# Kernel optimization log

Hardware: AMD Instinct MI355X
Metric: run time of the kernel (lower is better)

The kernel has to match this reference:

```python
import jax, jax.numpy as jnp
import numpy as np
import math

D_MODEL = 512
N_HEADS = 8
MAX_SEQ_LEN = 4096
DENSITY = 0.3


def _make_random_mask(key, seq_len, density=DENSITY):
    # rand < density, symmetrized via (m + m.T)/2, clamped to [0,1], diag = 1
    u = jax.random.uniform(key, (seq_len, seq_len), dtype=jnp.float32)
    m = (u < density).astype(jnp.float32)
    m = jnp.clip((m + m.T) * 0.5, 0.0, 1.0)
    return m.at[jnp.diag_indices(seq_len)].set(1.0)


def setup_inputs() -> dict:
    key = jax.random.key(0)
    ks = jax.random.split(key, 10)
    B, T, C = 2, 4096, D_MODEL
    scale = 1.0 / math.sqrt(C)
    x = jax.random.normal(ks[0], (B, T, C), dtype=jnp.float32)
    mask = _make_random_mask(ks[1], MAX_SEQ_LEN)[:T, :T]
    # Linear weights stored as (in, out): y = x @ W + b
    Wq = jax.random.normal(ks[2], (C, C), dtype=jnp.float32) * scale
    Wk = jax.random.normal(ks[3], (C, C), dtype=jnp.float32) * scale
    Wv = jax.random.normal(ks[4], (C, C), dtype=jnp.float32) * scale
    Wo = jax.random.normal(ks[5], (C, C), dtype=jnp.float32) * scale
    bq = jax.random.normal(ks[6], (C,), dtype=jnp.float32) * scale
    bk = jax.random.normal(ks[7], (C,), dtype=jnp.float32) * scale
    bv = jax.random.normal(ks[8], (C,), dtype=jnp.float32) * scale
    bo = jax.random.normal(ks[9], (C,), dtype=jnp.float32) * scale
    return {"x": x, "mask": mask, "Wq": Wq, "bq": bq, "Wk": Wk, "bk": bk,
            "Wv": Wv, "bv": bv, "Wo": Wo, "bo": bo}


def reference(x, mask, Wq, bq, Wk, bk, Wv, bv, Wo, bo):
    B, T, C = x.shape
    H = N_HEADS
    dk = C // H
    q = (x @ Wq + bq).reshape(B, T, H, dk)
    k = (x @ Wk + bk).reshape(B, T, H, dk)
    v = (x @ Wv + bv).reshape(B, T, H, dk)
    # scores: [B, H, T, T]
    attn = jnp.einsum('bthd,bshd->bhts', q, k) / math.sqrt(dk)
    attn = attn * mask[None, None, :, :]  # multiplicative mask PRE-softmax
    p = jax.nn.softmax(attn, axis=-1)
    out = jnp.einsum('bhts,bshd->bthd', p, v).reshape(B, T, C)
    return out @ Wo + bo
```

## Files before the change

kernel.cpp:

```cpp
#include <hip/hip_runtime.h>
#include <math.h>

#define D_MODEL 512
#define N_HEADS 8
#define DK 64

typedef __attribute__((ext_vector_type(8))) short short8;
typedef __attribute__((ext_vector_type(4))) float f32x4;

typedef __attribute__((address_space(1))) const unsigned as1_uint;
typedef __attribute__((address_space(3))) unsigned as3_uint;

__device__ __forceinline__ unsigned short f2bf(float f) {
    unsigned u = __builtin_bit_cast(unsigned, f);
    u = (u + 0x7fff + ((u >> 16) & 1)) >> 16;
    return (unsigned short)u;
}

__global__ __launch_bounds__(256) void cvt_x_kernel(const float* __restrict__ x,
                                                    unsigned short* __restrict__ xb, int n8)
{
    int i = blockIdx.x * 256 + threadIdx.x;
    if (i >= n8) return;
    float4 a = ((const float4*)x)[i * 2];
    float4 b = ((const float4*)x)[i * 2 + 1];
    short8 o;
    o[0] = f2bf(a.x); o[1] = f2bf(a.y); o[2] = f2bf(a.z); o[3] = f2bf(a.w);
    o[4] = f2bf(b.x); o[5] = f2bf(b.y); o[6] = f2bf(b.z); o[7] = f2bf(b.w);
    ((short8*)xb)[i] = o;
}

__global__ __launch_bounds__(256) void cvt_mask_kernel(const float* __restrict__ m,
                                                       unsigned char* __restrict__ mu, int n4)
{
    int i = blockIdx.x * 256 + threadIdx.x;
    if (i >= n4) return;
    float4 v = ((const float4*)m)[i];
    uchar4 o = { (unsigned char)(v.x * 2.0f + 0.5f),
                 (unsigned char)(v.y * 2.0f + 0.5f),
                 (unsigned char)(v.z * 2.0f + 0.5f),
                 (unsigned char)(v.w * 2.0f + 0.5f) };
    ((uchar4*)mu)[i] = o;
}

__global__ __launch_bounds__(256) void cvt_wt_kernel(const float* __restrict__ W,
                                                     unsigned short* __restrict__ Wt)
{
    __shared__ float tile[64][65];
    int t = threadIdx.x;
    int c0 = blockIdx.x * 64;
    int r0 = blockIdx.y * 64;
    #pragma unroll
    for (int i = 0; i < 16; i++) {
        int e = i * 256 + t, r = e >> 6, c = e & 63;
        tile[c][r] = W[(size_t)(r0 + r) * D_MODEL + c0 + c];
    }
    __syncthreads();
    #pragma unroll
    for (int i = 0; i < 16; i++) {
        int e = i * 256 + t, n = e >> 6, kk = e & 63;
        Wt[(size_t)(c0 + n) * D_MODEL + r0 + kk] = f2bf(tile[n][kk]);
    }
}

template<int MODE>
__global__ __launch_bounds__(512) void gemm_mfma_kernel(
    const unsigned short* __restrict__ A, const unsigned short* __restrict__ Bt,
    const float* __restrict__ bias, void* __restrict__ outp, int M, int T)
{
    constexpr int K = D_MODEL;
    __shared__ unsigned short As[2][128 * 32];
    __shared__ unsigned short Bs[2][128 * 32];
    int t = threadIdx.x;
    int lane = t & 63, w = t >> 6;
    int ql = lane & 15, kg = lane >> 4;
    int m0 = blockIdx.y * 128, n0 = blockIdx.x * 128;
    int wm = w >> 2, wn = w & 3;

    const unsigned short* srcA = A + (size_t)(m0 + (t >> 2)) * K + (t & 3) * 8;
    const unsigned short* srcB = Bt + (size_t)(n0 + (t >> 2)) * K + (t & 3) * 8;

    f32x4 acc[4][2];
    #pragma unroll
    for (int i = 0; i < 4; i++)
        #pragma unroll
        for (int j = 0; j < 2; j++) { f32x4 z = {0.f, 0.f, 0.f, 0.f}; acc[i][j] = z; }

    constexpr int NIT = K / 32;
    int cur = 0;
    __builtin_amdgcn_global_load_lds((as1_uint*)(srcA),
        (as3_uint*)((char*)&As[0][0] + w * 1024), 16, 0, 0);
    __builtin_amdgcn_global_load_lds((as1_uint*)(srcB),
        (as3_uint*)((char*)&Bs[0][0] + w * 1024), 16, 0, 0);
    __syncthreads();

    for (int it = 0; it < NIT; ++it) {
        if (it + 1 < NIT) {
            int k0 = (it + 1) * 32;
            __builtin_amdgcn_global_load_lds((as1_uint*)(srcA + k0),
                (as3_uint*)((char*)&As[cur ^ 1][0] + w * 1024), 16, 0, 0);
            __builtin_amdgcn_global_load_lds((as1_uint*)(srcB + k0),
                (as3_uint*)((char*)&Bs[cur ^ 1][0] + w * 1024), 16, 0, 0);
        }
        short8 af[4], bfr[2];
        #pragma unroll
        for (int fm = 0; fm < 4; fm++)
            af[fm] = *(const short8*)((const char*)&As[cur][0] + (wm * 64 + fm * 16 + ql) * 64 + kg * 16);
        #pragma unroll
        for (int fn = 0; fn < 2; fn++)
            bfr[fn] = *(const short8*)((const char*)&Bs[cur][0] + (wn * 32 + fn * 16 + ql) * 64 + kg * 16);
        #pragma unroll
        for (int fm = 0; fm < 4; fm++)
            #pragma unroll
            for (int fn = 0; fn < 2; fn++) {
                if (MODE == 3)
                    acc[fm][fn] = __builtin_amdgcn_mfma_f32_16x16x32_bf16(bfr[fn], af[fm], acc[fm][fn], 0, 0, 0);
                else
                    acc[fm][fn] = __builtin_amdgcn_mfma_f32_16x16x32_bf16(af[fm], bfr[fn], acc[fm][fn], 0, 0, 0);
            }
        __syncthreads();
        cur ^= 1;
    }

    #pragma unroll
    for (int fm = 0; fm < 4; fm++) {
        #pragma unroll
        for (int fn = 0; fn < 2; fn++) {
            if (MODE == 3) {
                int m = m0 + wm * 64 + fm * 16 + ql;
                int b = m / T, tt = m % T;
                #pragma unroll
                for (int r = 0; r < 4; r++) {
                    int n = n0 + wn * 32 + fn * 16 + kg * 4 + r;
                    float val = acc[fm][fn][r] + bias[n];
                    int h = n >> 6, d = n & 63;
                    ((unsigned short*)outp)[((size_t)(b * N_HEADS + h) * DK + d) * T + tt] = f2bf(val);
                }
            } else {
                int n = n0 + wn * 32 + fn * 16 + ql;
                float bn = bias[n];
                #pragma unroll
                for (int r = 0; r < 4; r++) {
                    int m = m0 + wm * 64 + fm * 16 + kg * 4 + r;
                    float val = acc[fm][fn][r] + bn;
                    if (MODE == 0) {
                        ((float*)outp)[(size_t)m * D_MODEL + n] = val;
                    } else {
                        if (MODE == 1) val *= 0.0625f * 1.44269504089f;
                        int b = m / T, tt = m % T;
                        int h = n >> 6, d = n & 63;
                        ((unsigned short*)outp)[((size_t)(b * N_HEADS + h) * T + tt) * DK + d] = f2bf(val);
                    }
                }
            }
        }
    }
}

__global__ __launch_bounds__(256) void attn_mfma_kernel(
    const unsigned short* __restrict__ q, const unsigned short* __restrict__ k,
    const unsigned short* __restrict__ v, const unsigned char* __restrict__ mu,
    unsigned short* __restrict__ out, int B, int T)
{
    __shared__ unsigned short Ks[2][64 * 64];
    __shared__ unsigned short Vt[2][64 * 64];
    __shared__ unsigned short Ps[4][32 * 64];

    int t = threadIdx.x;
    int lane = t & 63, w = t >> 6;
    int ql = lane & 15, kg = lane >> 4;
    int bh = blockIdx.x;
    int qt = blockIdx.y;
    int h = bh & (N_HEADS - 1), b = bh >> 3;
    int qr0 = qt * 128;

    const char* kbase = (const char*)(k + (size_t)bh * T * DK);
    const char* vbase = (const char*)(v + (size_t)bh * DK * T);

    int lin0 = w * 1024 + lane * 16;
    int lin1 = 4096 + lin0;
    int row0 = lin0 >> 7, row1 = lin1 >> 7;
    int sw0 = (row0 & 7) << 4, sw1 = (row1 & 7) << 4;
    const char* gK0 = kbase + (lin0 ^ sw0);
    const char* gK1 = kbase + (lin1 ^ sw1);
    const char* gV0 = vbase + (size_t)row0 * (2 * T) + ((lin0 & 127) ^ sw0);
    const char* gV1 = vbase + (size_t)row1 * (2 * T) + ((lin1 & 127) ^ sw1);

    short8 qfr[2][2];
    #pragma unroll
    for (int qf = 0; qf < 2; qf++) {
        const unsigned short* qrow = q + ((size_t)bh * T + qr0 + w * 32 + qf * 16 + ql) * DK + kg * 8;
        qfr[qf][0] = *(const short8*)(qrow);
        qfr[qf][1] = *(const short8*)(qrow + 32);
    }

    const unsigned char* mrow0 = mu + (size_t)(qr0 + w * 32 + ql) * T + kg * 4;
    const unsigned char* mrow1 = mrow0 + (size_t)16 * T;

    f32x4 oacc[2][4];
    #pragma unroll
    for (int qf = 0; qf < 2; qf++)
        #pragma unroll
        for (int c = 0; c < 4; c++) { f32x4 z = {0.f, 0.f, 0.f, 0.f}; oacc[qf][c] = z; }
    float lacc0 = 0.f, lacc1 = 0.f;

    unsigned mcur0[4], mcur1[4];
    #pragma unroll
    for (int c = 0; c < 4; c++) {
        mcur0[c] = *(const unsigned*)(mrow0 + c * 16);
        mcur1[c] = *(const unsigned*)(mrow1 + c * 16);
    }
    __builtin_amdgcn_global_load_lds((as1_uint*)gK0, (as3_uint*)((char*)&Ks[0][0] + w * 1024), 16, 0, 0);
    __builtin_amdgcn_global_load_lds((as1_uint*)gK1, (as3_uint*)((char*)&Ks[0][0] + 4096 + w * 1024), 16, 0, 0);
    __builtin_amdgcn_global_load_lds((as1_uint*)gV0, (as3_uint*)((char*)&Vt[0][0] + w * 1024), 16, 0, 0);
    __builtin_amdgcn_global_load_lds((as1_uint*)gV1, (as3_uint*)((char*)&Vt[0][0] + 4096 + w * 1024), 16, 0, 0);

    int ntiles = T / 64;
    for (int kt = 0; kt < ntiles; kt++) {
        __syncthreads();
        int cur = kt & 1;
        bool havenext = (kt + 1) < ntiles;

        unsigned mnxt0[4], mnxt1[4];
        if (havenext) {
            const unsigned char* mp0 = mrow0 + (size_t)(kt + 1) * 64;
            const unsigned char* mp1 = mrow1 + (size_t)(kt + 1) * 64;
            #pragma unroll
            for (int c = 0; c < 4; c++) {
                mnxt0[c] = *(const unsigned*)(mp0 + c * 16);
                mnxt1[c] = *(const unsigned*)(mp1 + c * 16);
            }
            size_t ko = (size_t)(kt + 1) * 8192;
            size_t vo = (size_t)(kt + 1) * 128;
            __builtin_amdgcn_global_load_lds((as1_uint*)(gK0 + ko),
                (as3_uint*)((char*)&Ks[cur ^ 1][0] + w * 1024), 16, 0, 0);
            __builtin_amdgcn_global_load_lds((as1_uint*)(gK1 + ko),
                (as3_uint*)((char*)&Ks[cur ^ 1][0] + 4096 + w * 1024), 16, 0, 0);
            __builtin_amdgcn_global_load_lds((as1_uint*)(gV0 + vo),
                (as3_uint*)((char*)&Vt[cur ^ 1][0] + w * 1024), 16, 0, 0);
            __builtin_amdgcn_global_load_lds((as1_uint*)(gV1 + vo),
                (as3_uint*)((char*)&Vt[cur ^ 1][0] + 4096 + w * 1024), 16, 0, 0);
        }

        f32x4 sacc[2][4];
        #pragma unroll
        for (int qf = 0; qf < 2; qf++)
            #pragma unroll
            for (int c = 0; c < 4; c++) { f32x4 z = {0.f, 0.f, 0.f, 0.f}; sacc[qf][c] = z; }
        __builtin_amdgcn_s_setprio(1);
        #pragma unroll
        for (int ks = 0; ks < 2; ks++) {
            #pragma unroll
            for (int c = 0; c < 4; c++) {
                int row = c * 16 + ql;
                short8 kf = *(const short8*)((const char*)&Ks[cur][0] +
                            ((row * 128 + ks * 64 + kg * 16) ^ ((row & 7) << 4)));
                sacc[0][c] = __builtin_amdgcn_mfma_f32_16x16x32_bf16(kf, qfr[0][ks], sacc[0][c], 0, 0, 0);
                sacc[1][c] = __builtin_amdgcn_mfma_f32_16x16x32_bf16(kf, qfr[1][ks], sacc[1][c], 0, 0, 0);
            }
        }
        __builtin_amdgcn_s_setprio(0);

        #pragma unroll
        for (int c = 0; c < 4; c++) {
            unsigned mw = mcur0[c];
            float p0 = __builtin_amdgcn_exp2f(sacc[0][c][0] * (float)(mw & 0xffu));
            float p1 = __builtin_amdgcn_exp2f(sacc[0][c][1] * (float)((mw >> 8) & 0xffu));
            float p2 = __builtin_amdgcn_exp2f(sacc[0][c][2] * (float)((mw >> 16) & 0xffu));
            float p3 = __builtin_amdgcn_exp2f(sacc[0][c][3] * (float)(mw >> 24));
            lacc0 += (p0 + p1) + (p2 + p3);
            unsigned lo, hi;
            asm("v_cvt_pk_bf16_f32 %0, %1, %2" : "=v"(lo) : "v"(p0), "v"(p1));
            asm("v_cvt_pk_bf16_f32 %0, %1, %2" : "=v"(hi) : "v"(p2), "v"(p3));
            int byteoff = (ql * 128 + (c * 16 + kg * 4) * 2) ^ ((ql & 7) << 4);
            uint2 pr = { lo, hi };
            *(uint2*)((char*)&Ps[w][0] + byteoff) = pr;

            unsigned nw = mcur1[c];
            float q0 = __builtin_amdgcn_exp2f(sacc[1][c][0] * (float)(nw & 0xffu));
            float q1 = __builtin_amdgcn_exp2f(sacc[1][c][1] * (float)((nw >> 8) & 0xffu));
            float q2 = __builtin_amdgcn_exp2f(sacc[1][c][2] * (float)((nw >> 16) & 0xffu));
            float q3 = __builtin_amdgcn_exp2f(sacc[1][c][3] * (float)(nw >> 24));
            lacc1 += (q0 + q1) + (q2 + q3);
            unsigned lo1, hi1;
            asm("v_cvt_pk_bf16_f32 %0, %1, %2" : "=v"(lo1) : "v"(q0), "v"(q1));
            asm("v_cvt_pk_bf16_f32 %0, %1, %2" : "=v"(hi1) : "v"(q2), "v"(q3));
            uint2 pr1 = { lo1, hi1 };
            *(uint2*)((char*)&Ps[w][0] + 2048 + byteoff) = pr1;
        }

        __builtin_amdgcn_s_setprio(1);
        #pragma unroll
        for (int ks = 0; ks < 2; ks++) {
            int pboff = (ql * 128 + ks * 64 + kg * 16) ^ ((ql & 7) << 4);
            short8 pa0 = *(const short8*)((const char*)&Ps[w][0] + pboff);
            short8 pa1 = *(const short8*)((const char*)&Ps[w][0] + 2048 + pboff);
            #pragma unroll
            for (int c2 = 0; c2 < 4; c2++) {
                int rowd = c2 * 16 + ql;
                short8 vb = *(const short8*)((const char*)&Vt[cur][0] +
                            ((rowd * 128 + ks * 64 + kg * 16) ^ ((rowd & 7) << 4)));
                oacc[0][c2] = __builtin_amdgcn_mfma_f32_16x16x32_bf16(pa0, vb, oacc[0][c2], 0, 0, 0);
                oacc[1][c2] = __builtin_amdgcn_mfma_f32_16x16x32_bf16(pa1, vb, oacc[1][c2], 0, 0, 0);
            }
        }
        __builtin_amdgcn_s_setprio(0);

        if (havenext) {
            #pragma unroll
            for (int c = 0; c < 4; c++) { mcur0[c] = mnxt0[c]; mcur1[c] = mnxt1[c]; }
        }
    }

    lacc0 += __shfl_xor(lacc0, 16, 64);
    lacc0 += __shfl_xor(lacc0, 32, 64);
    lacc1 += __shfl_xor(lacc1, 16, 64);
    lacc1 += __shfl_xor(lacc1, 32, 64);
    #pragma unroll
    for (int qf = 0; qf < 2; qf++) {
        float la = qf ? lacc1 : lacc0;
        #pragma unroll
        for (int r = 0; r < 4; r++) {
            float linv = 1.0f / __shfl(la, kg * 4 + r, 64);
            size_t rowo = ((size_t)b * T + qr0 + w * 32 + qf * 16 + kg * 4 + r) * D_MODEL + h * DK;
            #pragma unroll
            for (int c2 = 0; c2 < 4; c2++)
                out[rowo + c2 * 16 + ql] = f2bf(oacc[qf][c2][r] * linv);
        }
    }
}

extern "C" void kernel_launch(void* const* d_in, const int* in_sizes, int n_in,
                              void* d_out, int out_size, void* d_ws, size_t ws_size,
                              hipStream_t stream) {
    const float* x    = (const float*)d_in[0];
    const float* mask = (const float*)d_in[1];
    const float* Wq   = (const float*)d_in[2];
    const float* bq   = (const float*)d_in[3];
    const float* Wk   = (const float*)d_in[4];
    const float* bk   = (const float*)d_in[5];
    const float* Wv   = (const float*)d_in[6];
    const float* bv   = (const float*)d_in[7];
    const float* Wo   = (const float*)d_in[8];
    const float* bo   = (const float*)d_in[9];

    int T = (int)(sqrt((double)in_sizes[1]) + 0.5);
    int C = D_MODEL;
    int B = in_sizes[0] / (T * C);
    int M = B * T;

    size_t MK = (size_t)M * C;
    unsigned short* xb  = (unsigned short*)d_ws;
    unsigned short* Wtq = xb + MK;
    unsigned short* Wtk = Wtq + (size_t)C * C;
    unsigned short* Wtv = Wtk + (size_t)C * C;
    unsigned short* Wto = Wtv + (size_t)C * C;
    unsigned short* qb  = Wto + (size_t)C * C;
    unsigned short* kb  = qb + MK;
    unsigned short* vb  = kb + MK;
    unsigned short* attb = vb + MK;
    unsigned char*  mu  = (unsigned char*)(attb + MK);

    int n8 = (int)(MK / 8);
    cvt_x_kernel<<<(n8 + 255) / 256, 256, 0, stream>>>(x, xb, n8);
    int n4 = T * T / 4;
    cvt_mask_kernel<<<(n4 + 255) / 256, 256, 0, stream>>>(mask, mu, n4);
    dim3 wtg(C / 64, C / 64, 1);
    cvt_wt_kernel<<<wtg, 256, 0, stream>>>(Wq, Wtq);
    cvt_wt_kernel<<<wtg, 256, 0, stream>>>(Wk, Wtk);
    cvt_wt_kernel<<<wtg, 256, 0, stream>>>(Wv, Wtv);
    cvt_wt_kernel<<<wtg, 256, 0, stream>>>(Wo, Wto);

    dim3 gg(C / 128, M / 128, 1);
    gemm_mfma_kernel<1><<<gg, 512, 0, stream>>>(xb, Wtq, bq, qb, M, T);
    gemm_mfma_kernel<2><<<gg, 512, 0, stream>>>(xb, Wtk, bk, kb, M, T);
    gemm_mfma_kernel<3><<<gg, 512, 0, stream>>>(xb, Wtv, bv, vb, M, T);

    dim3 ga(B * N_HEADS, T / 128, 1);
    attn_mfma_kernel<<<ga, 256, 0, stream>>>(qb, kb, vb, mu, attb, B, T);

    gemm_mfma_kernel<0><<<gg, 512, 0, stream>>>(attb, Wto, bo, d_out, M, T);
}
```

Baseline: 225.1 us.

## Split attention KV range across two blocks, fuse QKV GEMMs, defer PV

Fuses the three Q/K/V projection GEMMs into one launch. This relies on the Wtq/Wtk/Wtv buffers sitting next to each other in the workspace, so they act as one 1536-wide weight. Splits the attention key range into two halves along a new grid dimension, which doubles the block count from 512 to 1024 for better CU occupancy. Each half writes unnormalized fp32 partial outputs and row sums, and a new merge kernel combines and normalizes them. The V tile is now single-buffered and the PV product is software-pipelined one tile behind QK. The cost is extra fp32 partial traffic (about 16MB written and read back) and one additional launch.

After: 258.0 us. +14.6%, slower.

```diff
diff --git a/kernel.cpp b/kernel.cpp
--- a/kernel.cpp
+++ b/kernel.cpp
@@ -4,6 +4,7 @@
 #define D_MODEL 512
 #define N_HEADS 8
 #define DK 64
+#define QSCALE (0.0625f * 1.44269504089f)
 
 typedef __attribute__((ext_vector_type(8))) short short8;
 typedef __attribute__((ext_vector_type(4))) float f32x4;
@@ -63,10 +64,11 @@
     }
 }
 
-template<int MODE>
-__global__ __launch_bounds__(512) void gemm_mfma_kernel(
-    const unsigned short* __restrict__ A, const unsigned short* __restrict__ Bt,
-    const float* __restrict__ bias, void* __restrict__ outp, int M, int T)
+__global__ __launch_bounds__(512) void gemm_qkv_kernel(
+    const unsigned short* __restrict__ A, const unsigned short* __restrict__ Wt,
+    const float* __restrict__ bq, const float* __restrict__ bk, const float* __restrict__ bv,
+    unsigned short* __restrict__ qb, unsigned short* __restrict__ kb,
+    unsigned short* __restrict__ vb, int M, int T)
 {
     constexpr int K = D_MODEL;
     __shared__ unsigned short As[2][128 * 32];
@@ -76,9 +78,10 @@
     int ql = lane & 15, kg = lane >> 4;
     int m0 = blockIdx.y * 128, n0 = blockIdx.x * 128;
     int wm = w >> 2, wn = w & 3;
+    bool vmode = (n0 >= 1024);
 
     const unsigned short* srcA = A + (size_t)(m0 + (t >> 2)) * K + (t & 3) * 8;
-    const unsigned short* srcB = Bt + (size_t)(n0 + (t >> 2)) * K + (t & 3) * 8;
+    const unsigned short* srcB = Wt + (size_t)(n0 + (t >> 2)) * K + (t & 3) * 8;
 
     f32x4 acc[4][2];
     #pragma unroll
@@ -109,15 +112,19 @@
         #pragma unroll
         for (int fn = 0; fn < 2; fn++)
             bfr[fn] = *(const short8*)((const char*)&Bs[cur][0] + (wn * 32 + fn * 16 + ql) * 64 + kg * 16);
-        #pragma unroll
-        for (int fm = 0; fm < 4; fm++)
-            #pragma unroll
-            for (int fn = 0; fn < 2; fn++) {
-                if (MODE == 3)
+        if (vmode) {
+            #pragma unroll
+            for (int fm = 0; fm < 4; fm++)
+                #pragma unroll
+                for (int fn = 0; fn < 2; fn++)
                     acc[fm][fn] = __builtin_amdgcn_mfma_f32_16x16x32_bf16(bfr[fn], af[fm], acc[fm][fn], 0, 0, 0);
-                else
+        } else {
+            #pragma unroll
+            for (int fm = 0; fm < 4; fm++)
+                #pragma unroll
+                for (int fn = 0; fn < 2; fn++)
                     acc[fm][fn] = __builtin_amdgcn_mfma_f32_16x16x32_bf16(af[fm], bfr[fn], acc[fm][fn], 0, 0, 0);
-            }
+        }
         __syncthreads();
         cur ^= 1;
     }
@@ -126,32 +133,100 @@
     for (int fm = 0; fm < 4; fm++) {
         #pragma unroll
         for (int fn = 0; fn < 2; fn++) {
-            if (MODE == 3) {
+            if (vmode) {
                 int m = m0 + wm * 64 + fm * 16 + ql;
                 int b = m / T, tt = m % T;
                 #pragma unroll
                 for (int r = 0; r < 4; r++) {
-                    int n = n0 + wn * 32 + fn * 16 + kg * 4 + r;
-                    float val = acc[fm][fn][r] + bias[n];
+                    int n = (n0 - 1024) + wn * 32 + fn * 16 + kg * 4 + r;
+                    float val = acc[fm][fn][r] + bv[n];
                     int h = n >> 6, d = n & 63;
-                    ((unsigned short*)outp)[((size_t)(b * N_HEADS + h) * DK + d) * T + tt] = f2bf(val);
+                    vb[((size_t)(b * N_HEADS + h) * DK + d) * T + tt] = f2bf(val);
                 }
             } else {
                 int n = n0 + wn * 32 + fn * 16 + ql;
-                float bn = bias[n];
+                int nn = n & 511;
+                bool isq = (n0 < 512);
+                float bn = isq ? bq[nn] : bk[nn];
+                unsigned short* dst = isq ? qb : kb;
+                int h = nn >> 6, d = nn & 63;
                 #pragma unroll
                 for (int r = 0; r < 4; r++) {
                     int m = m0 + wm * 64 + fm * 16 + kg * 4 + r;
+                    int b = m / T, tt = m % T;
                     float val = acc[fm][fn][r] + bn;
-                    if (MODE == 0) {
-                        ((float*)outp)[(size_t)m * D_MODEL + n] = val;
-                    } else {
-                        if (MODE == 1) val *= 0.0625f * 1.44269504089f;
-                        int b = m / T, tt = m % T;
-                        int h = n >> 6, d = n & 63;
-                        ((unsigned short*)outp)[((size_t)(b * N_HEADS + h) * T + tt) * DK + d] = f2bf(val);
-                    }
+                    if (isq) val *= QSCALE;
+                    dst[((size_t)(b * N_HEADS + h) * T + tt) * DK + d] = f2bf(val);
                 }
+            }
+        }
+    }
+}
+
+__global__ __launch_bounds__(512) void gemm_out_kernel(
+    const unsigned short* __restrict__ A, const unsigned short* __restrict__ Bt,
+    const float* __restrict__ bias, float* __restrict__ outp, int M)
+{
+    constexpr int K = D_MODEL;
+    __shared__ unsigned short As[2][128 * 32];
+    __shared__ unsigned short Bs[2][128 * 32];
+    int t = threadIdx.x;
+    int lane = t & 63, w = t >> 6;
+    int ql = lane & 15, kg = lane >> 4;
+    int m0 = blockIdx.y * 128, n0 = blockIdx.x * 128;
+    int wm = w >> 2, wn = w & 3;
+
+    const unsigned short* srcA = A + (size_t)(m0 + (t >> 2)) * K + (t & 3) * 8;
+    const unsigned short* srcB = Bt + (size_t)(n0 + (t >> 2)) * K + (t & 3) * 8;
+
+    f32x4 acc[4][2];
+    #pragma unroll
+    for (int i = 0; i < 4; i++)
+        #pragma unroll
+        for (int j = 0; j < 2; j++) { f32x4 z = {0.f, 0.f, 0.f, 0.f}; acc[i][j] = z; }
+
+    constexpr int NIT = K / 32;
+    int cur = 0;
+    __builtin_amdgcn_global_load_lds((as1_uint*)(srcA),
+        (as3_uint*)((char*)&As[0][0] + w * 1024), 16, 0, 0);
+    __builtin_amdgcn_global_load_lds((as1_uint*)(srcB),
+        (as3_uint*)((char*)&Bs[0][0] + w * 1024), 16, 0, 0);
+    __syncthreads();
+
+    for (int it = 0; it < NIT; ++it) {
+        if (it + 1 < NIT) {
+            int k0 = (it + 1) * 32;
+            __builtin_amdgcn_global_load_lds((as1_uint*)(srcA + k0),
+                (as3_uint*)((char*)&As[cur ^ 1][0] + w * 1024), 16, 0, 0);
+            __builtin_amdgcn_global_load_lds((as1_uint*)(srcB + k0),
+                (as3_uint*)((char*)&Bs[cur ^ 1][0] + w * 1024), 16, 0, 0);
+        }
+        short8 af[4], bfr[2];
+        #pragma unroll
+        for (int fm = 0; fm < 4; fm++)
+            af[fm] = *(const short8*)((const char*)&As[cur][0] + (wm * 64 + fm * 16 + ql) * 64 + kg * 16);
+        #pragma unroll
+        for (int fn = 0; fn < 2; fn++)
+            bfr[fn] = *(const short8*)((const char*)&Bs[cur][0] + (wn * 32 + fn * 16 + ql) * 64 + kg * 16);
+        #pragma unroll
+        for (int fm = 0; fm < 4; fm++)
+            #pragma unroll
+            for (int fn = 0; fn < 2; fn++)
+                acc[fm][fn] = __builtin_amdgcn_mfma_f32_16x16x32_bf16(af[fm], bfr[fn], acc[fm][fn], 0, 0, 0);
+        __syncthreads();
+        cur ^= 1;
+    }
+
+    #pragma unroll
+    for (int fm = 0; fm < 4; fm++) {
+        #pragma unroll
+        for (int fn = 0; fn < 2; fn++) {
+            int n = n0 + wn * 32 + fn * 16 + ql;
+            float bn = bias[n];
+            #pragma unroll
+            for (int r = 0; r < 4; r++) {
+                int m = m0 + wm * 64 + fm * 16 + kg * 4 + r;
+                outp[(size_t)m * D_MODEL + n] = acc[fm][fn][r] + bn;
             }
         }
     }
@@ -160,22 +235,25 @@
 __global__ __launch_bounds__(256) void attn_mfma_kernel(
     const unsigned short* __restrict__ q, const unsigned short* __restrict__ k,
     const unsigned short* __restrict__ v, const unsigned char* __restrict__ mu,
-    unsigned short* __restrict__ out, int B, int T)
+    float* __restrict__ opart, float* __restrict__ lpart, int B, int T)
 {
     __shared__ unsigned short Ks[2][64 * 64];
-    __shared__ unsigned short Vt[2][64 * 64];
+    __shared__ unsigned short Vt[64 * 64];
     __shared__ unsigned short Ps[4][32 * 64];
 
     int t = threadIdx.x;
     int lane = t & 63, w = t >> 6;
     int ql = lane & 15, kg = lane >> 4;
-    int bh = blockIdx.x;
-    int qt = blockIdx.y;
+    int bh = blockIdx.x, qt = blockIdx.y, z = blockIdx.z;
     int h = bh & (N_HEADS - 1), b = bh >> 3;
     int qr0 = qt * 128;
-
-    const char* kbase = (const char*)(k + (size_t)bh * T * DK);
-    const char* vbase = (const char*)(v + (size_t)bh * DK * T);
+    int Th = T >> 1;
+    int kv0 = z * Th;
+    int nt = Th / 64;
+    int M = B * T;
+
+    const char* kbase = (const char*)(k + ((size_t)bh * T + kv0) * DK);
+    const char* vbase = (const char*)(v + (size_t)bh * DK * T + kv0);
 
     int lin0 = w * 1024 + lane * 16;
     int lin1 = 4096 + lin0;
@@ -194,14 +272,14 @@
         qfr[qf][1] = *(const short8*)(qrow + 32);
     }
 
-    const unsigned char* mrow0 = mu + (size_t)(qr0 + w * 32 + ql) * T + kg * 4;
+    const unsigned char* mrow0 = mu + (size_t)(qr0 + w * 32 + ql) * T + kv0 + kg * 4;
     const unsigned char* mrow1 = mrow0 + (size_t)16 * T;
 
     f32x4 oacc[2][4];
     #pragma unroll
     for (int qf = 0; qf < 2; qf++)
         #pragma unroll
-        for (int c = 0; c < 4; c++) { f32x4 z = {0.f, 0.f, 0.f, 0.f}; oacc[qf][c] = z; }
+        for (int c = 0; c < 4; c++) { f32x4 zz = {0.f, 0.f, 0.f, 0.f}; oacc[qf][c] = zz; }
     float lacc0 = 0.f, lacc1 = 0.f;
 
     unsigned mcur0[4], mcur1[4];
@@ -212,14 +290,11 @@
     }
     __builtin_amdgcn_global_load_lds((as1_uint*)gK0, (as3_uint*)((char*)&Ks[0][0] + w * 1024), 16, 0, 0);
     __builtin_amdgcn_global_load_lds((as1_uint*)gK1, (as3_uint*)((char*)&Ks[0][0] + 4096 + w * 1024), 16, 0, 0);
-    __builtin_amdgcn_global_load_lds((as1_uint*)gV0, (as3_uint*)((char*)&Vt[0][0] + w * 1024), 16, 0, 0);
-    __builtin_amdgcn_global_load_lds((as1_uint*)gV1, (as3_uint*)((char*)&Vt[0][0] + 4096 + w * 1024), 16, 0, 0);
-
-    int ntiles = T / 64;
-    for (int kt = 0; kt < ntiles; kt++) {
+
+    for (int kt = 0; kt < nt; kt++) {
         __syncthreads();
         int cur = kt & 1;
-        bool havenext = (kt + 1) < ntiles;
+        bool havenext = (kt + 1) < nt;
 
         unsigned mnxt0[4], mnxt1[4];
         if (havenext) {
@@ -231,22 +306,48 @@
                 mnxt1[c] = *(const unsigned*)(mp1 + c * 16);
             }
             size_t ko = (size_t)(kt + 1) * 8192;
-            size_t vo = (size_t)(kt + 1) * 128;
             __builtin_amdgcn_global_load_lds((as1_uint*)(gK0 + ko),
                 (as3_uint*)((char*)&Ks[cur ^ 1][0] + w * 1024), 16, 0, 0);
             __builtin_amdgcn_global_load_lds((as1_uint*)(gK1 + ko),
                 (as3_uint*)((char*)&Ks[cur ^ 1][0] + 4096 + w * 1024), 16, 0, 0);
+        }
+
+        if (kt > 0) {
+            __builtin_amdgcn_s_setprio(1);
+            #pragma unroll
+            for (int ks = 0; ks < 2; ks++) {
+                int pboff = (ql * 128 + ks * 64 + kg * 16) ^ ((ql & 7) << 4);
+                short8 pa0 = *(const short8*)((const char*)&Ps[w][0] + pboff);
+                short8 pa1 = *(const short8*)((const char*)&Ps[w][0] + 2048 + pboff);
+                #pragma unroll
+                for (int c2 = 0; c2 < 4; c2++) {
+                    int rowd = c2 * 16 + ql;
+                    short8 vb = *(const short8*)((const char*)Vt +
+                                ((rowd * 128 + ks * 64 + kg * 16) ^ ((rowd & 7) << 4)));
+                    oacc[0][c2] = __builtin_amdgcn_mfma_f32_16x16x32_bf16(pa0, vb, oacc[0][c2], 0, 0, 0);
+                    oacc[1][c2] = __builtin_amdgcn_mfma_f32_16x16x32_bf16(pa1, vb, oacc[1][c2], 0, 0, 0);
+                }
+            }
+            __builtin_amdgcn_s_setprio(0);
+        }
+
+        __builtin_amdgcn_sched_barrier(0);
+        __builtin_amdgcn_s_barrier();
+        __builtin_amdgcn_sched_barrier(0);
+
+        {
+            size_t vo = (size_t)kt * 128;
             __builtin_amdgcn_global_load_lds((as1_uint*)(gV0 + vo),
-                (as3_uint*)((char*)&Vt[cur ^ 1][0] + w * 1024), 16, 0, 0);
+                (as3_uint*)((char*)Vt + w * 1024), 16, 0, 0);
             __builtin_amdgcn_global_load_lds((as1_uint*)(gV1 + vo),
-                (as3_uint*)((char*)&Vt[cur ^ 1][0] + 4096 + w * 1024), 16, 0, 0);
+                (as3_uint*)((char*)Vt + 4096 + w * 1024), 16, 0, 0);
         }
 
         f32x4 sacc[2][4];
         #pragma unroll
         for (int qf = 0; qf < 2; qf++)
             #pragma unroll
-            for (int c = 0; c < 4; c++) { f32x4 z = {0.f, 0.f, 0.f, 0.f}; sacc[qf][c] = z; }
+            for (int c = 0; c < 4; c++) { f32x4 zz = {0.f, 0.f, 0.f, 0.f}; sacc[qf][c] = zz; }
         __builtin_amdgcn_s_setprio(1);
         #pragma unroll
         for (int ks = 0; ks < 2; ks++) {
@@ -289,45 +390,74 @@
             *(uint2*)((char*)&Ps[w][0] + 2048 + byteoff) = pr1;
         }
 
-        __builtin_amdgcn_s_setprio(1);
-        #pragma unroll
-        for (int ks = 0; ks < 2; ks++) {
-            int pboff = (ql * 128 + ks * 64 + kg * 16) ^ ((ql & 7) << 4);
-            short8 pa0 = *(const short8*)((const char*)&Ps[w][0] + pboff);
-            short8 pa1 = *(const short8*)((const char*)&Ps[w][0] + 2048 + pboff);
-            #pragma unroll
-            for (int c2 = 0; c2 < 4; c2++) {
-                int rowd = c2 * 16 + ql;
-                short8 vb = *(const short8*)((const char*)&Vt[cur][0] +
-                            ((rowd * 128 + ks * 64 + kg * 16) ^ ((rowd & 7) << 4)));
-                oacc[0][c2] = __builtin_amdgcn_mfma_f32_16x16x32_bf16(pa0, vb, oacc[0][c2], 0, 0, 0);
-                oacc[1][c2] = __builtin_amdgcn_mfma_f32_16x16x32_bf16(pa1, vb, oacc[1][c2], 0, 0, 0);
-            }
-        }
-        __builtin_amdgcn_s_setprio(0);
-
         if (havenext) {
             #pragma unroll
             for (int c = 0; c < 4; c++) { mcur0[c] = mnxt0[c]; mcur1[c] = mnxt1[c]; }
         }
     }
+
+    __syncthreads();
+    __builtin_amdgcn_s_setprio(1);
+    #pragma unroll
+    for (int ks = 0; ks < 2; ks++) {
+        int pboff = (ql * 128 + ks * 64 + kg * 16) ^ ((ql & 7) << 4);
+        short8 pa0 = *(const short8*)((const char*)&Ps[w][0] + pboff);
+        short8 pa1 = *(const short8*)((const char*)&Ps[w][0] + 2048 + pboff);
+        #pragma unroll
+        for (int c2 = 0; c2 < 4; c2++) {
+            int rowd = c2 * 16 + ql;
+            short8 vb = *(const short8*)((const char*)Vt +
+                        ((rowd * 128 + ks * 64 + kg * 16) ^ ((rowd & 7) << 4)));
+            oacc[0][c2] = __builtin_amdgcn_mfma_f32_16x16x32_bf16(pa0, vb, oacc[0][c2], 0, 0, 0);
+            oacc[1][c2] = __builtin_amdgcn_mfma_f32_16x16x32_bf16(pa1, vb, oacc[1][c2], 0, 0, 0);
+        }
+    }
+    __builtin_amdgcn_s_setprio(0);
 
     lacc0 += __shfl_xor(lacc0, 16, 64);
     lacc0 += __shfl_xor(lacc0, 32, 64);
     lacc1 += __shfl_xor(lacc1, 16, 64);
     lacc1 += __shfl_xor(lacc1, 32, 64);
+    if (kg == 0) {
+        lpart[((size_t)z * 16 + bh) * T + qr0 + w * 32 + ql] = lacc0;
+        lpart[((size_t)z * 16 + bh) * T + qr0 + w * 32 + 16 + ql] = lacc1;
+    }
     #pragma unroll
     for (int qf = 0; qf < 2; qf++) {
-        float la = qf ? lacc1 : lacc0;
         #pragma unroll
         for (int r = 0; r < 4; r++) {
-            float linv = 1.0f / __shfl(la, kg * 4 + r, 64);
-            size_t rowo = ((size_t)b * T + qr0 + w * 32 + qf * 16 + kg * 4 + r) * D_MODEL + h * DK;
+            size_t rowo = ((size_t)z * M + (size_t)b * T + qr0 + w * 32 + qf * 16 + kg * 4 + r) * D_MODEL + h * DK;
+            f32x4* oa = &oacc[qf][0];
             #pragma unroll
             for (int c2 = 0; c2 < 4; c2++)
-                out[rowo + c2 * 16 + ql] = f2bf(oacc[qf][c2][r] * linv);
-        }
-    }
+                opart[rowo + c2 * 16 + ql] = oa[c2][r];
+        }
+    }
+}
+
+__global__ __launch_bounds__(256) void merge_kernel(
+    const float* __restrict__ opart, const float* __restrict__ lpart,
+    unsigned short* __restrict__ attb, int M, int T)
+{
+    int t = threadIdx.x;
+    int lane = t & 63;
+    int m = blockIdx.x * 4 + (t >> 6);
+    int b = m / T, tt = m % T;
+    int h = lane >> 3;
+    size_t o0 = (size_t)m * D_MODEL + lane * 8;
+    const float4* pa = (const float4*)(opart + o0);
+    const float4* pb = (const float4*)(opart + (size_t)M * D_MODEL + o0);
+    float4 a0 = pa[0], a1 = pa[1];
+    float4 b0 = pb[0], b1 = pb[1];
+    float l0 = lpart[(size_t)(b * N_HEADS + h) * T + tt];
+    float l1 = lpart[(size_t)16 * T + (size_t)(b * N_HEADS + h) * T + tt];
+    float r = 1.0f / (l0 + l1);
+    short8 o;
+    o[0] = f2bf((a0.x + b0.x) * r); o[1] = f2bf((a0.y + b0.y) * r);
+    o[2] = f2bf((a0.z + b0.z) * r); o[3] = f2bf((a0.w + b0.w) * r);
+    o[4] = f2bf((a1.x + b1.x) * r); o[5] = f2bf((a1.y + b1.y) * r);
+    o[6] = f2bf((a1.z + b1.z) * r); o[7] = f2bf((a1.w + b1.w) * r);
+    *(short8*)(attb + o0) = o;
 }
 
 extern "C" void kernel_launch(void* const* d_in, const int* in_sizes, int n_in,
@@ -360,6 +490,8 @@
     unsigned short* vb  = kb + MK;
     unsigned short* attb = vb + MK;
     unsigned char*  mu  = (unsigned char*)(attb + MK);
+    float* opart = (float*)(mu + (size_t)T * T);
+    float* lpart = opart + 2 * (size_t)M * C;
 
     int n8 = (int)(MK / 8);
     cvt_x_kernel<<<(n8 + 255) / 256, 256, 0, stream>>>(x, xb, n8);
@@ -371,13 +503,14 @@
     cvt_wt_kernel<<<wtg, 256, 0, stream>>>(Wv, Wtv);
     cvt_wt_kernel<<<wtg, 256, 0, stream>>>(Wo, Wto);
 
+    dim3 gq(3 * C / 128, M / 128, 1);
+    gemm_qkv_kernel<<<gq, 512, 0, stream>>>(xb, Wtq, bq, bk, bv, qb, kb, vb, M, T);
+
+    dim3 ga(B * N_HEADS, T / 128, 2);
+    attn_mfma_kernel<<<ga, 256, 0, stream>>>(qb, kb, vb, mu, opart, lpart, B, T);
+
+    merge_kernel<<<M / 4, 256, 0, stream>>>(opart, lpart, attb, M, T);
+
     dim3 gg(C / 128, M / 128, 1);
-    gemm_mfma_kernel<1><<<gg, 512, 0, stream>>>(xb, Wtq, bq, qb, M, T);
-    gemm_mfma_kernel<2><<<gg, 512, 0, stream>>>(xb, Wtk, bk, kb, M, T);
-    gemm_mfma_kernel<3><<<gg, 512, 0, stream>>>(xb, Wtv, bv, vb, M, T);
-
-    dim3 ga(B * N_HEADS, T / 128, 1);
-    attn_mfma_kernel<<<ga, 256, 0, stream>>>(qb, kb, vb, mu, attb, B, T);
-
-    gemm_mfma_kernel<0><<<gg, 512, 0, stream>>>(attb, Wto, bo, d_out, M, T);
-}
+    gemm_out_kernel<<<gg, 512, 0, stream>>>(attb, Wto, bo, (float*)d_out, M);
+}
```
